# Optimization experiments

Hardware: AMD Instinct MI355X
Metric: run time of the kernel (lower is better)

The kernel has to match this reference:

```python
import jax, jax.numpy as jnp
import numpy as np

B, T, D, H = 4, 2048, 1024, 16
DH = D // H  # head dim = 64
FLOAT_MIN = jnp.finfo(jnp.float32).min


def setup_inputs() -> dict:
    key = jax.random.key(0)
    k1, k2, k3 = jax.random.split(key, 3)
    scale = 1.0 / np.sqrt(D)
    return {
        "x": jax.random.normal(k1, (B, T, D), dtype=jnp.float32),
        "W_qkv": jax.random.normal(k2, (D, 3 * D), dtype=jnp.float32) * scale,
        "b_qkv": jnp.zeros((3 * D,), dtype=jnp.float32),
        "W_out": jax.random.normal(k3, (D, D), dtype=jnp.float32) * scale,
        "b_out": jnp.zeros((D,), dtype=jnp.float32),
        "mask": jnp.ones((B, T, T), dtype=jnp.float32),
    }


def _split_heads(t):
    # [B, T, D] -> [B, H, T, DH]
    b, s, _ = t.shape
    return t.reshape(b, s, H, DH).transpose(0, 2, 1, 3)


def reference(x, W_qkv, b_qkv, W_out, b_out, mask):
    # fused QKV projection (Conv1D kernel-size 1 == per-position dense)
    qkv = jnp.einsum("btd,de->bte", x, W_qkv) + b_qkv
    q, k, v = jnp.split(qkv, 3, axis=-1)
    q = _split_heads(q) * (DH ** -0.5)  # [B, H, T, DH]
    k = _split_heads(k)
    v = _split_heads(v)
    # scores [B, H, Tq, Tk]
    dot = jnp.einsum("bhqd,bhkd->bhqk", q, k)
    m = mask[:, None, :, :]  # expand over heads
    dot = dot * m + (1.0 - m) * FLOAT_MIN
    attn = jax.nn.softmax(dot, axis=-1)
    ctx = jnp.einsum("bhqk,bhkd->bhqd", attn, v)  # [B, H, T, DH]
    combined = ctx.transpose(0, 2, 1, 3).reshape(x.shape[0], x.shape[1], D)
    out = jnp.einsum("btd,de->bte", combined, W_out) + b_out
    return out
```

## Files before the change

### kernel.cpp

```cpp
#include <hip/hip_runtime.h>

typedef short bf16x8 __attribute__((ext_vector_type(8)));
typedef float f32x4 __attribute__((ext_vector_type(4)));
typedef float f32x16 __attribute__((ext_vector_type(16)));
typedef unsigned short u16x8 __attribute__((ext_vector_type(8)));

#define DEVI __device__ __forceinline__

static constexpr int T_ = 2048;

DEVI unsigned short f2bf(float f) {
  unsigned int x = __builtin_bit_cast(unsigned int, f);
  x += 0x7fffu + ((x >> 16) & 1u);
  return (unsigned short)(x >> 16);
}

DEVI unsigned int cvtpk(float lo, float hi2) {
  unsigned int r;
  asm("v_cvt_pk_bf16_f32 %0, %1, %2" : "=v"(r) : "v"(lo), "v"(hi2));
  return r;
}

DEVI float exp2_raw(float x) {
  float r;
  asm("v_exp_f32 %0, %1" : "=v"(r) : "v"(x));
  return r;
}

DEVI int swz23(int r) {
  const int d = ((r >> 2) ^ (r >> 3)) & 1;
  return r ^ (d << 2) ^ (d << 3);
}

DEVI bf16x8 mkfrag(unsigned a, unsigned b, unsigned c, unsigned d) {
  union { unsigned u[4]; bf16x8 v; } x;
  x.u[0] = a; x.u[1] = b; x.u[2] = c; x.u[3] = d;
  return x.v;
}

DEVI void gl2lds16(const void* g, const void* l) {
  __builtin_amdgcn_global_load_lds(
      (const __attribute__((address_space(1))) void*)g,
      (__attribute__((address_space(3))) void*)l, 16, 0, 0);
}

__global__ __launch_bounds__(256) void k_cvt_bf16(const float* __restrict__ in,
                                                  unsigned short* __restrict__ out) {
  size_t i = ((size_t)blockIdx.x * 256 + threadIdx.x) * 8;
  float4 a = *(const float4*)(in + i);
  float4 b = *(const float4*)(in + i + 4);
  u16x8 o;
  o[0] = f2bf(a.x); o[1] = f2bf(a.y); o[2] = f2bf(a.z); o[3] = f2bf(a.w);
  o[4] = f2bf(b.x); o[5] = f2bf(b.y); o[6] = f2bf(b.z); o[7] = f2bf(b.w);
  *(u16x8*)(out + i) = o;
}

__global__ __launch_bounds__(256) void k_mask_scan(const uint4* __restrict__ m,
                                                   unsigned int* __restrict__ flag) {
  const unsigned int ONE = 0x3f800000u;
  size_t i0 = ((size_t)blockIdx.x * 256 + threadIdx.x) * 8;
  bool ok = true;
#pragma unroll
  for (int i = 0; i < 8; ++i) {
    uint4 v = m[i0 + i];
    ok &= (v.x == ONE) & (v.y == ONE) & (v.z == ONE) & (v.w == ONE);
  }
  if (!ok) atomicAnd(flag, 0u);
}

template <int R, int C>
__global__ __launch_bounds__(256) void k_transpose_cvt(const float* __restrict__ in,
                                                       unsigned short* __restrict__ out) {
  __shared__ unsigned short t[64][65];
  const int c0 = blockIdx.x * 64, r0 = blockIdx.y * 64;
  const int cc = threadIdx.x & 63, r4 = threadIdx.x >> 6;
#pragma unroll
  for (int i = 0; i < 16; ++i) {
    int rr = i * 4 + r4;
    t[rr][cc] = f2bf(in[(size_t)(r0 + rr) * C + c0 + cc]);
  }
  __syncthreads();
#pragma unroll
  for (int i = 0; i < 16; ++i) {
    int rr = i * 4 + r4;
    out[(size_t)(c0 + rr) * R + r0 + cc] = t[cc][rr];
  }
}

__global__ __launch_bounds__(256) void k_transpose_v(const unsigned short* __restrict__ V,
                                                     unsigned short* __restrict__ Vt) {
  __shared__ unsigned short t[64][65];
  const int t0 = blockIdx.x * 64;
  const size_t bh = blockIdx.y;
  const unsigned short* src = V + (bh * T_ + t0) * 64;
  unsigned short* dst = Vt + bh * 64 * T_ + t0;
  const int cc = threadIdx.x & 63, r4 = threadIdx.x >> 6;
#pragma unroll
  for (int i = 0; i < 16; ++i) {
    int rr = i * 4 + r4;
    t[rr][cc] = src[(size_t)rr * 64 + cc];
  }
  __syncthreads();
#pragma unroll
  for (int i = 0; i < 16; ++i) {
    int rr = i * 4 + r4;
    dst[(size_t)rr * T_ + cc] = t[cc][rr];
  }
}

template <int EPI, int NT>
__global__ __launch_bounds__(512, 2) void k_gemm8(
    const unsigned short* __restrict__ A, const unsigned short* __restrict__ Bt,
    const float* __restrict__ bias,
    unsigned short* __restrict__ qo, unsigned short* __restrict__ ko2,
    unsigned short* __restrict__ vo, float* __restrict__ fo) {
  __shared__ unsigned short As[3][256 * 64];
  __shared__ unsigned short Bs[3][128 * 64];
  const int tid = threadIdx.x, lane = tid & 63, w = tid >> 6;
  const int wm = w >> 1, wn = w & 1;
  const int g = lane >> 4, c0 = lane & 15;

  const int flat = blockIdx.x;
  const int work = (flat & 7) * ((32 * NT) >> 3) + (flat >> 3);
  const int m0 = (work / NT) * 256, n0 = (work % NT) * 128;

  f32x4 acc[4][4] = {};

  const int rs = tid >> 3, chs = tid & 7;
  const int lwb = w * 512;

  auto stageK = [&](int buf, int kt) {
    const unsigned short* sa = A + (size_t)m0 * 1024 + kt * 64;
    const unsigned short* sb = Bt + (size_t)n0 * 1024 + kt * 64;
    unsigned short* da = &As[buf][0];
    unsigned short* db = &Bs[buf][0];
#pragma unroll
    for (int j = 0; j < 4; ++j) {
      const int row = rs + j * 64;
      const int ch = chs ^ (row & 7);
      gl2lds16(sa + (size_t)row * 1024 + ch * 8, da + j * 4096 + lwb);
    }
#pragma unroll
    for (int j = 0; j < 2; ++j) {
      const int row = rs + j * 64;
      const int ch = chs ^ (row & 7);
      gl2lds16(sb + (size_t)row * 1024 + ch * 8, db + j * 4096 + lwb);
    }
  };

  stageK(0, 0);
  stageK(1, 1);
  asm volatile("s_waitcnt vmcnt(6)" ::: "memory");
  __builtin_amdgcn_s_barrier();

  int cb = 0;
  for (int k = 0; k < 16; ++k) {
    bf16x8 af[4][2], bfv[4][2];
#pragma unroll
    for (int mf = 0; mf < 4; ++mf) {
      const int row = wm * 64 + mf * 16 + c0;
#pragma unroll
      for (int kk = 0; kk < 2; ++kk) {
        const int ch = (kk * 4 + g) ^ (row & 7);
        af[mf][kk] = *(const bf16x8*)&As[cb][row * 64 + ch * 8];
      }
    }
#pragma unroll
    for (int nf = 0; nf < 4; ++nf) {
      const int row = wn * 64 + nf * 16 + c0;
#pragma unroll
      for (int kk = 0; kk < 2; ++kk) {
        const int ch = (kk * 4 + g) ^ (row & 7);
        bfv[nf][kk] = *(const bf16x8*)&Bs[cb][row * 64 + ch * 8];
      }
    }
    if (k + 2 < 16) stageK((cb + 2) % 3, k + 2);
    __builtin_amdgcn_s_barrier();
    asm volatile("s_waitcnt lgkmcnt(0)" ::: "memory");
    __builtin_amdgcn_sched_barrier(0);
#pragma unroll
    for (int kk = 0; kk < 2; ++kk)
#pragma unroll
      for (int mf = 0; mf < 4; ++mf)
#pragma unroll
        for (int nf = 0; nf < 4; ++nf)
          acc[mf][nf] = __builtin_amdgcn_mfma_f32_16x16x32_bf16(af[mf][kk], bfv[nf][kk], acc[mf][nf], 0, 0, 0);
    if (k <= 13)      asm volatile("s_waitcnt vmcnt(6)" ::: "memory");
    else if (k == 14) asm volatile("s_waitcnt vmcnt(0)" ::: "memory");
    __builtin_amdgcn_s_barrier();
    cb = (cb == 2) ? 0 : cb + 1;
  }

#pragma unroll
  for (int mf = 0; mf < 4; ++mf) {
#pragma unroll
    for (int nf = 0; nf < 4; ++nf) {
      const int n = n0 + wn * 64 + nf * 16 + c0;
      const float bv = bias[n];
#pragma unroll
      for (int r = 0; r < 4; ++r) {
        const int m = m0 + wm * 64 + mf * 16 + g * 4 + r;
        float v = acc[mf][nf][r] + bv;
        if constexpr (EPI == 0) {
          const int sel = n >> 10, hd = n & 1023;
          const int h = hd >> 6, d = hd & 63;
          const int b = m >> 11, t = m & 2047;
          const size_t off = ((size_t)((b * 16 + h) * 2048 + t)) * 64 + d;
          if (sel == 0)       qo[off] = f2bf(v * 0.125f);
          else if (sel == 1)  ko2[off] = f2bf(v);
          else                vo[off] = f2bf(v);
        } else {
          fo[(size_t)m * 1024 + n] = v;
        }
      }
    }
  }
}

__global__ __launch_bounds__(256, 4) void k_attn(
    const unsigned short* __restrict__ Q, const unsigned short* __restrict__ Kg_,
    const unsigned short* __restrict__ Vt, const float* __restrict__ mask,
    const unsigned int* __restrict__ maskflag,
    unsigned short* __restrict__ ctx) {
  __shared__ unsigned short Ks[2][64 * 64];
  __shared__ unsigned short Vs[2][64 * 64];
  const int tid = threadIdx.x, lane = tid & 63, w = tid >> 6;
  const int q = lane & 31, hi = lane >> 5;

  const int flat = blockIdx.x + 16 * blockIdx.y + 256 * blockIdx.z;
  const int work = (flat & 7) * 128 + (flat >> 3);
  const int qb = work & 15;
  const int bh_i = work >> 4;
  const int h = bh_i & 15, b = bh_i >> 4;
  const int t0 = qb * 128;
  const size_t bh = (size_t)bh_i;

  const unsigned short* Qg = Q + (bh * 2048 + t0 + w * 32 + q) * 64;
  const unsigned short* Kg = Kg_ + bh * 2048 * 64;
  const unsigned short* Vg = Vt + bh * 64 * 2048;
  const float* Mg = mask + (size_t)b * 2048 * 2048;
  const bool allones = (*maskflag != 0u);

  bf16x8 qf[4];
#pragma unroll
  for (int kd = 0; kd < 4; ++kd)
    qf[kd] = *(const bf16x8*)(Qg + kd * 16 + hi * 8);

  f32x16 ot[2] = {};
  float mrun = -__builtin_inff(), lrun = 0.f;

  const int s0 = tid, s1 = tid + 256;
  const int kr0 = s0 >> 3, kc0 = (s0 & 7) ^ (kr0 & 7);
  const int kr1 = s1 >> 3, kc1 = (s1 & 7) ^ (kr1 & 7);
  const int kp0 = swz23(kr0), kp1 = swz23(kr1);
  const int ldsb0 = w * 512, ldsb1 = w * 512 + 2048;

  auto stageKV = [&](int buf, int kt) {
    gl2lds16(Kg + (size_t)(kt * 64 + kp0) * 64 + kc0 * 8, &Ks[buf][ldsb0]);
    gl2lds16(Kg + (size_t)(kt * 64 + kp1) * 64 + kc1 * 8, &Ks[buf][ldsb1]);
    gl2lds16(Vg + (size_t)kr0 * 2048 + kt * 64 + kc0 * 8, &Vs[buf][ldsb0]);
    gl2lds16(Vg + (size_t)kr1 * 2048 + kt * 64 + kc1 * 8, &Vs[buf][ldsb1]);
  };

  stageKV(0, 0);
  __syncthreads();
  int cur = 0;
  const float MINF = -3.402823466e38f;
  const float L2E = 1.4426950408889634f;

  for (int kt = 0; kt < 32; ++kt) {
    if (kt + 1 < 32) stageKV(cur ^ 1, kt + 1);

    f32x16 st[2] = {};
#pragma unroll
    for (int mt2 = 0; mt2 < 2; ++mt2) {
      __builtin_amdgcn_s_setprio(1);
#pragma unroll
      for (int kd = 0; kd < 4; ++kd) {
        const int row = mt2 * 32 + q;
        const int ch = (2 * kd + hi) ^ (row & 7);
        bf16x8 kf = *(const bf16x8*)&Ks[cur][row * 64 + ch * 8];
        st[mt2] = __builtin_amdgcn_mfma_f32_32x32x16_bf16(kf, qf[kd], st[mt2], 0, 0, 0);
      }
      __builtin_amdgcn_s_setprio(0);
    }

    if (!allones) {
      const int qg = t0 + w * 32 + q;
#pragma unroll
      for (int mt2 = 0; mt2 < 2; ++mt2)
#pragma unroll
        for (int r = 0; r < 16; ++r) {
          const int kg = kt * 64 + mt2 * 32 +
                         (r & 3) + 4 * ((r >> 2) & 1) + 8 * hi + 16 * (r >> 3);
          const float mv = Mg[(size_t)qg * 2048 + kg];
          st[mt2][r] = st[mt2][r] * mv + (1.f - mv) * MINF;
        }
    }

    float g4[8];
#pragma unroll
    for (int i = 0; i < 4; ++i) {
      g4[i]     = fmaxf(fmaxf(fmaxf(st[0][4 * i], st[0][4 * i + 1]), st[0][4 * i + 2]), st[0][4 * i + 3]);
      g4[i + 4] = fmaxf(fmaxf(fmaxf(st[1][4 * i], st[1][4 * i + 1]), st[1][4 * i + 2]), st[1][4 * i + 3]);
    }
    float r1 = fmaxf(fmaxf(g4[0], g4[1]), g4[2]);
    float r2 = fmaxf(fmaxf(g4[3], g4[4]), g4[5]);
    float r3 = fmaxf(fmaxf(g4[6], g4[7]), r1);
    float tmax = fmaxf(r2, r3);
    tmax = fmaxf(tmax, __shfl_xor(tmax, 32));
    const bool defer = (__all(tmax <= mrun + 8.f) != 0);
    float alpha = 1.f;
    if (!defer) {
      const float mnew = fmaxf(mrun, tmax);
      alpha = exp2_raw((mrun - mnew) * L2E);
      mrun = mnew;
    }
    const float mL2 = mrun * L2E;
#pragma unroll
    for (int mt2 = 0; mt2 < 2; ++mt2)
#pragma unroll
      for (int i = 0; i < 16; ++i)
        st[mt2][i] = exp2_raw(st[mt2][i] * L2E - mL2);
    float s8[8];
#pragma unroll
    for (int i = 0; i < 8; ++i)
      s8[i] = (st[0][i] + st[0][i + 8]) + (st[1][i] + st[1][i + 8]);
    float s4a = s8[0] + s8[4], s4b = s8[1] + s8[5];
    float s4c = s8[2] + s8[6], s4d = s8[3] + s8[7];
    float ps = (s4a + s4b) + (s4c + s4d);
    ps += __shfl_xor(ps, 32);
    lrun = lrun * alpha + ps;
    if (!defer) {
#pragma unroll
      for (int dt = 0; dt < 2; ++dt)
#pragma unroll
        for (int i = 0; i < 16; ++i) ot[dt][i] *= alpha;
    }

    bf16x8 pf[4];
#pragma unroll
    for (int mt2 = 0; mt2 < 2; ++mt2) {
      unsigned int pw[8];
#pragma unroll
      for (int i = 0; i < 8; ++i) pw[i] = cvtpk(st[mt2][2 * i], st[mt2][2 * i + 1]);
      pf[2 * mt2]     = mkfrag(pw[0], pw[1], pw[2], pw[3]);
      pf[2 * mt2 + 1] = mkfrag(pw[4], pw[5], pw[6], pw[7]);
    }

#pragma unroll
    for (int dt = 0; dt < 2; ++dt) {
      __builtin_amdgcn_s_setprio(1);
#pragma unroll
      for (int kt2 = 0; kt2 < 4; ++kt2) {
        const int row = dt * 32 + q;
        const int ch = (2 * kt2 + hi) ^ (row & 7);
        bf16x8 vf = *(const bf16x8*)&Vs[cur][row * 64 + ch * 8];
        ot[dt] = __builtin_amdgcn_mfma_f32_32x32x16_bf16(vf, pf[kt2], ot[dt], 0, 0, 0);
      }
      __builtin_amdgcn_s_setprio(0);
    }

    __syncthreads();
    cur ^= 1;
  }

  const int qg = t0 + w * 32 + q;
  const float rl = 1.f / lrun;
  unsigned short* cp = ctx + ((size_t)b * 2048 + qg) * 1024 + h * 64;
#pragma unroll
  for (int dt = 0; dt < 2; ++dt) {
#pragma unroll
    for (int rg = 0; rg < 4; ++rg) {
      const int d0 = dt * 32 + rg * 8 + hi * 4;
      ushort4 o;
      o.x = f2bf(ot[dt][rg * 4 + 0] * rl);
      o.y = f2bf(ot[dt][rg * 4 + 1] * rl);
      o.z = f2bf(ot[dt][rg * 4 + 2] * rl);
      o.w = f2bf(ot[dt][rg * 4 + 3] * rl);
      *(ushort4*)(cp + d0) = o;
    }
  }
}

extern "C" void kernel_launch(void* const* d_in, const int* in_sizes, int n_in,
                              void* d_out, int out_size, void* d_ws, size_t ws_size,
                              hipStream_t stream) {
  (void)in_sizes; (void)n_in; (void)out_size; (void)ws_size;
  const float* x    = (const float*)d_in[0];
  const float* Wqkv = (const float*)d_in[1];
  const float* bqkv = (const float*)d_in[2];
  const float* Wout = (const float*)d_in[3];
  const float* bout = (const float*)d_in[4];
  const float* mask = (const float*)d_in[5];
  float* out = (float*)d_out;
  char* ws = (char*)d_ws;

  const size_t SZ_BTD = (size_t)8192 * 1024 * 2;
  unsigned short* xb  = (unsigned short*)(ws);
  unsigned short* Wqt = (unsigned short*)(ws + SZ_BTD);
  unsigned short* Wot = (unsigned short*)(ws + SZ_BTD + 6291456);
  unsigned short* Qb  = (unsigned short*)(ws + SZ_BTD + 8388608);
  unsigned short* Kb  = (unsigned short*)(ws + SZ_BTD + 8388608 + SZ_BTD);
  unsigned short* Vb  = (unsigned short*)(ws + SZ_BTD + 8388608 + 2 * SZ_BTD);
  unsigned short* Vtb = (unsigned short*)(ws + SZ_BTD + 8388608 + 3 * SZ_BTD);
  unsigned int* flag  = (unsigned int*)(ws + SZ_BTD + 8388608 + 4 * SZ_BTD);
  unsigned short* ctx = xb;

  hipMemsetAsync(flag, 1, 4, stream);
  k_mask_scan<<<2048, 256, 0, stream>>>((const uint4*)mask, flag);
  k_cvt_bf16<<<4096, 256, 0, stream>>>(x, xb);
  k_transpose_cvt<1024, 3072><<<dim3(48, 16), 256, 0, stream>>>(Wqkv, Wqt);
  k_transpose_cvt<1024, 1024><<<dim3(16, 16), 256, 0, stream>>>(Wout, Wot);
  k_gemm8<0, 24><<<768, 512, 0, stream>>>(xb, Wqt, bqkv, Qb, Kb, Vb, nullptr);
  k_transpose_v<<<dim3(32, 64), 256, 0, stream>>>(Vb, Vtb);
  k_attn<<<dim3(16, 16, 4), 256, 0, stream>>>(Qb, Kb, Vtb, mask, flag, ctx);
  k_gemm8<1, 8><<<256, 512, 0, stream>>>(ctx, Wot, bout, nullptr, nullptr, nullptr, out);
}
```

Measured before the change: 223.7 us.

## Split GEMM k-tile into two half-phases with interleaved staging and setprio

```diff
diff --git a/kernel.cpp b/kernel.cpp
--- a/kernel.cpp
+++ b/kernel.cpp
@@ -129,62 +129,82 @@
   const int rs = tid >> 3, chs = tid & 7;
   const int lwb = w * 512;
 
-  auto stageK = [&](int buf, int kt) {
+  auto stageHalf = [&](int buf, int kt, int half) {
     const unsigned short* sa = A + (size_t)m0 * 1024 + kt * 64;
     const unsigned short* sb = Bt + (size_t)n0 * 1024 + kt * 64;
     unsigned short* da = &As[buf][0];
     unsigned short* db = &Bs[buf][0];
-#pragma unroll
-    for (int j = 0; j < 4; ++j) {
+    const int ja = half * 2;
+#pragma unroll
+    for (int j = ja; j < ja + 2; ++j) {
       const int row = rs + j * 64;
       const int ch = chs ^ (row & 7);
       gl2lds16(sa + (size_t)row * 1024 + ch * 8, da + j * 4096 + lwb);
     }
-#pragma unroll
-    for (int j = 0; j < 2; ++j) {
-      const int row = rs + j * 64;
+    {
+      const int row = rs + half * 64;
       const int ch = chs ^ (row & 7);
-      gl2lds16(sb + (size_t)row * 1024 + ch * 8, db + j * 4096 + lwb);
+      gl2lds16(sb + (size_t)row * 1024 + ch * 8, db + half * 4096 + lwb);
     }
   };
 
-  stageK(0, 0);
-  stageK(1, 1);
+  stageHalf(0, 0, 0); stageHalf(0, 0, 1);
+  stageHalf(1, 1, 0); stageHalf(1, 1, 1);
   asm volatile("s_waitcnt vmcnt(6)" ::: "memory");
   __builtin_amdgcn_s_barrier();
 
   int cb = 0;
   for (int k = 0; k < 16; ++k) {
-    bf16x8 af[4][2], bfv[4][2];
+    const int nb = (cb + 2) % 3;
+    bf16x8 af0[4], bf0[4];
 #pragma unroll
     for (int mf = 0; mf < 4; ++mf) {
       const int row = wm * 64 + mf * 16 + c0;
-#pragma unroll
-      for (int kk = 0; kk < 2; ++kk) {
-        const int ch = (kk * 4 + g) ^ (row & 7);
-        af[mf][kk] = *(const bf16x8*)&As[cb][row * 64 + ch * 8];
-      }
+      const int ch = g ^ (row & 7);
+      af0[mf] = *(const bf16x8*)&As[cb][row * 64 + ch * 8];
     }
 #pragma unroll
     for (int nf = 0; nf < 4; ++nf) {
       const int row = wn * 64 + nf * 16 + c0;
-#pragma unroll
-      for (int kk = 0; kk < 2; ++kk) {
-        const int ch = (kk * 4 + g) ^ (row & 7);
-        bfv[nf][kk] = *(const bf16x8*)&Bs[cb][row * 64 + ch * 8];
-      }
-    }
-    if (k + 2 < 16) stageK((cb + 2) % 3, k + 2);
+      const int ch = g ^ (row & 7);
+      bf0[nf] = *(const bf16x8*)&Bs[cb][row * 64 + ch * 8];
+    }
+    if (k + 2 < 16) stageHalf(nb, k + 2, 0);
     __builtin_amdgcn_s_barrier();
     asm volatile("s_waitcnt lgkmcnt(0)" ::: "memory");
     __builtin_amdgcn_sched_barrier(0);
-#pragma unroll
-    for (int kk = 0; kk < 2; ++kk)
-#pragma unroll
-      for (int mf = 0; mf < 4; ++mf)
-#pragma unroll
-        for (int nf = 0; nf < 4; ++nf)
-          acc[mf][nf] = __builtin_amdgcn_mfma_f32_16x16x32_bf16(af[mf][kk], bfv[nf][kk], acc[mf][nf], 0, 0, 0);
+    __builtin_amdgcn_s_setprio(1);
+#pragma unroll
+    for (int mf = 0; mf < 4; ++mf)
+#pragma unroll
+      for (int nf = 0; nf < 4; ++nf)
+        acc[mf][nf] = __builtin_amdgcn_mfma_f32_16x16x32_bf16(af0[mf], bf0[nf], acc[mf][nf], 0, 0, 0);
+    __builtin_amdgcn_s_setprio(0);
+    __builtin_amdgcn_s_barrier();
+    bf16x8 af1[4], bf1[4];
+#pragma unroll
+    for (int mf = 0; mf < 4; ++mf) {
+      const int row = wm * 64 + mf * 16 + c0;
+      const int ch = (4 + g) ^ (row & 7);
+      af1[mf] = *(const bf16x8*)&As[cb][row * 64 + ch * 8];
+    }
+#pragma unroll
+    for (int nf = 0; nf < 4; ++nf) {
+      const int row = wn * 64 + nf * 16 + c0;
+      const int ch = (4 + g) ^ (row & 7);
+      bf1[nf] = *(const bf16x8*)&Bs[cb][row * 64 + ch * 8];
+    }
+    if (k + 2 < 16) stageHalf(nb, k + 2, 1);
+    __builtin_amdgcn_s_barrier();
+    asm volatile("s_waitcnt lgkmcnt(0)" ::: "memory");
+    __builtin_amdgcn_sched_barrier(0);
+    __builtin_amdgcn_s_setprio(1);
+#pragma unroll
+    for (int mf = 0; mf < 4; ++mf)
+#pragma unroll
+      for (int nf = 0; nf < 4; ++nf)
+        acc[mf][nf] = __builtin_amdgcn_mfma_f32_16x16x32_bf16(af1[mf], bf1[nf], acc[mf][nf], 0, 0, 0);
+    __builtin_amdgcn_s_setprio(0);
     if (k <= 13)      asm volatile("s_waitcnt vmcnt(6)" ::: "memory");
     else if (k == 14) asm volatile("s_waitcnt vmcnt(0)" ::: "memory");
     __builtin_amdgcn_s_barrier();
```

Result: no change. 225.8 us (+0.9%).
